# Optimization experiments

Measured on AMD Instinct MI355X. Metric: run time of the kernel, lower is better.

Reference implementation:

```python
import jax, jax.numpy as jnp
import numpy as np

B, S, D, H = 4, 2048, 1024, 16
DK = D // H
THETA = 10000.0


def _rope(x, pos):
    # x: [..., S, DK]; interleaved-pair rotation as in the torch module
    dk = x.shape[-1]
    inv_freq = 1.0 / (THETA ** (jnp.arange(0, dk, 2, dtype=jnp.float32) / dk))  # [dk/2]
    freqs = pos.astype(jnp.float32)[:, None] * inv_freq  # [S, dk/2]
    cos, sin = jnp.cos(freqs), jnp.sin(freqs)
    xr = x.reshape(*x.shape[:-1], dk // 2, 2)
    x0, x1 = xr[..., 0], xr[..., 1]
    rot = jnp.stack([x0 * cos - x1 * sin, x0 * sin + x1 * cos], axis=-1)
    return rot.reshape(x.shape)


def setup_inputs() -> dict:
    key = jax.random.key(0)
    ks = jax.random.split(key, 5)
    scale = 0.02
    return {
        "x": jax.random.normal(ks[0], (B, S, D), dtype=jnp.float32),
        "Wq": jax.random.normal(ks[1], (D, D), dtype=jnp.float32) * scale,
        "Wk": jax.random.normal(ks[2], (D, D), dtype=jnp.float32) * scale,
        "Wv": jax.random.normal(ks[3], (D, D), dtype=jnp.float32) * scale,
        "Wo": jax.random.normal(ks[4], (D, D), dtype=jnp.float32) * scale,
    }


def reference(x, Wq, Wk, Wv, Wo):
    b, s, d = x.shape
    pos = jnp.arange(s)
    # projections (Linear with no bias, y = x @ W^T)
    q = jnp.einsum('bsd,ed->bse', x, Wq).reshape(b, s, H, DK).transpose(0, 2, 1, 3)
    k = jnp.einsum('bsd,ed->bse', x, Wk).reshape(b, s, H, DK).transpose(0, 2, 1, 3)
    v = jnp.einsum('bsd,ed->bse', x, Wv).reshape(b, s, H, DK).transpose(0, 2, 1, 3)
    q = _rope(q, pos)
    k = _rope(k, pos)
    scores = jnp.einsum('bhqd,bhkd->bhqk', q, k) / jnp.sqrt(jnp.float32(DK))
    causal = jnp.tril(jnp.ones((s, s), dtype=bool))
    scores = jnp.where(causal, scores, -jnp.inf)
    attn = jax.nn.softmax(scores, axis=-1)
    out = jnp.einsum('bhqk,bhkd->bhqd', attn, v)
    out = out.transpose(0, 2, 1, 3).reshape(b, s, d)
    return jnp.einsum('bsd,ed->bse', out, Wo)
```

## Files before the change

kernel.cpp:

```cpp
#include <hip/hip_runtime.h>

#define B_  4
#define S_  2048
#define D_  1024
#define H_  16
#define DK_ 64
#define BH_ (B_*H_)
#define L2E 1.44269504088896f

typedef __attribute__((ext_vector_type(8))) short bf16x8;
typedef __attribute__((ext_vector_type(4))) float f32x4;
typedef __attribute__((ext_vector_type(16))) float f32x16;
typedef __attribute__((ext_vector_type(4))) unsigned u32x4;
typedef unsigned short u16;

__device__ __forceinline__ u16 f2bf(float f){
  unsigned u = __builtin_bit_cast(unsigned, f);
  u += 0x7fffu + ((u >> 16) & 1u);
  return (u16)(u >> 16);
}
__device__ __forceinline__ float bf2f(u16 h){
  unsigned u = ((unsigned)h) << 16;
  return __builtin_bit_cast(float, u);
}

#define GLD16(g,l) __builtin_amdgcn_global_load_lds( \
    (const __attribute__((address_space(1))) void*)(g), \
    (__attribute__((address_space(3))) void*)(l), 16, 0, 0)

#define MFMA16(a,b,c) __builtin_amdgcn_mfma_f32_16x16x32_bf16((a),(b),(c),0,0,0)
#define MFMA32(a,b,c) __builtin_amdgcn_mfma_f32_32x32x16_bf16((a),(b),(c),0,0,0)

__global__ void cast_kernel(const float4* __restrict__ in, ushort4* __restrict__ out, int n4){
  int i = blockIdx.x*blockDim.x + threadIdx.x;
  int stride = gridDim.x*blockDim.x;
  for (; i < n4; i += stride){
    float4 v = in[i];
    ushort4 o;
    o.x = f2bf(v.x); o.y = f2bf(v.y); o.z = f2bf(v.z); o.w = f2bf(v.w);
    out[i] = o;
  }
}

__global__ void trig_kernel(float* __restrict__ ct, float* __restrict__ st){
  int t = blockIdx.x*blockDim.x + threadIdx.x;
  int i = t & 31, s = t >> 5;
  float expo = -(float)(2*i) * (1.0f/(float)DK_);
  float inv = powf(10000.0f, expo);
  float ang = (float)s * inv;
  ct[t] = cosf(ang);
  st[t] = sinf(ang);
}

template<int MODE>
__global__ __launch_bounds__(256, 2)
void gemm_bt(const u16* __restrict__ A,
             const u16* __restrict__ B0, const u16* __restrict__ B1, const u16* __restrict__ B2,
             u16* __restrict__ O0, u16* __restrict__ O1, u16* __restrict__ O2,
             float* __restrict__ Cf,
             const float* __restrict__ ct, const float* __restrict__ st, int K){
  __shared__ __align__(16) u16 lAB[2*128*64];
  u16* const lA = lAB;
  u16* const lB = lAB + 128*64;
  const u16* Bm = B0;
  u16* Om = O0;
  if (MODE == 0){
    if (blockIdx.z == 1){ Bm = B1; Om = O1; }
    else if (blockIdx.z == 2){ Bm = B2; Om = O2; }
  }
  const int m0 = blockIdx.y*128, n0 = blockIdx.x*128;
  const int tid = threadIdx.x, wave = tid>>6, lane = tid&63;
  const int wm = wave>>1, wn = wave&1;
  const int srow = lane>>3, scol = (lane&7)*8;

  f32x4 acc[4][4];
  #pragma unroll
  for (int m=0;m<4;++m)
    #pragma unroll
    for (int n=0;n<4;++n) acc[m][n] = (f32x4){0.f,0.f,0.f,0.f};

  #pragma unroll 1
  for (int k0 = 0; k0 < K; k0 += 64){
    #pragma unroll
    for (int j=0;j<4;++j){
      int rb = (wave*4 + j)*8;
      GLD16(A  + (size_t)(m0 + rb + srow)*K + k0 + scol, lA + rb*64);
      GLD16(Bm + (size_t)(n0 + rb + srow)*K + k0 + scol, lB + rb*64);
    }
    __syncthreads();
    #pragma unroll
    for (int kk=0;kk<2;++kk){
      bf16x8 af[4], bfr[4];
      #pragma unroll
      for (int m=0;m<4;++m) af[m]  = *(const bf16x8*)&lA[(wm*64 + m*16 + (lane&15))*64 + kk*32 + (lane>>4)*8];
      #pragma unroll
      for (int n=0;n<4;++n) bfr[n] = *(const bf16x8*)&lB[(wn*64 + n*16 + (lane&15))*64 + kk*32 + (lane>>4)*8];
      #pragma unroll
      for (int m=0;m<4;++m)
        #pragma unroll
        for (int n=0;n<4;++n)
          acc[m][n] = MFMA16(af[m], bfr[n], acc[m][n]);
    }
    __syncthreads();
  }

  if (MODE == 0 && blockIdx.z != 2){
    const float scale = (blockIdx.z == 0) ? 0.125f : 1.0f;
    #pragma unroll
    for (int m=0;m<4;++m){
      const int lr0 = wm*64 + m*16 + ((lane>>4)<<2);
      #pragma unroll
      for (int n=0;n<4;++n){
        const int lc = wn*64 + n*16 + (lane&15);
        #pragma unroll
        for (int r=0;r<4;++r){
          const int lr = lr0 + r;
          lAB[lr*128 + (lc ^ (((lr>>2)&7)<<4))] = f2bf(acc[m][n][r]);
        }
      }
    }
    __syncthreads();
    #pragma unroll
    for (int k=0;k<8;++k){
      const int cid = k*256 + tid;
      const int rr = cid >> 4, cc = cid & 15;
      bf16x8 v = *(const bf16x8*)&lAB[rr*128 + ((cc*8) ^ (((rr>>2)&7)<<4))];
      const int i = m0 + rr, bb = i >> 11, s = i & (S_-1);
      const int e0 = n0 + cc*8, h = e0 >> 6, dk0 = e0 & 63;
      const float4 c4 = *(const float4*)(ct + s*32 + (dk0>>1));
      const float4 s4 = *(const float4*)(st + s*32 + (dk0>>1));
      const float cc4[4] = {c4.x,c4.y,c4.z,c4.w};
      const float ss4[4] = {s4.x,s4.y,s4.z,s4.w};
      bf16x8 o;
      #pragma unroll
      for (int j=0;j<4;++j){
        const float x0 = bf2f((u16)v[2*j]);
        const float x1 = bf2f((u16)v[2*j+1]);
        o[2*j]   = (short)f2bf((x0*cc4[j] - x1*ss4[j])*scale);
        o[2*j+1] = (short)f2bf((x0*ss4[j] + x1*cc4[j])*scale);
      }
      *(bf16x8*)(Om + ((size_t)((bb*H_ + h)*S_ + s))*DK_ + dk0) = o;
    }
  } else {
    #pragma unroll
    for (int m=0;m<4;++m){
      const int rb = m0 + wm*64 + m*16 + ((lane>>4)<<2);
      #pragma unroll
      for (int n=0;n<4;++n){
        const int e = n0 + wn*64 + n*16 + (lane&15);
        if (MODE == 0){
          const int h = e>>6, dk = e&63;
          const int b = rb >> 11, s0 = rb & (S_-1);
          ushort4 w4;
          w4.x = f2bf(acc[m][n][0]); w4.y = f2bf(acc[m][n][1]);
          w4.z = f2bf(acc[m][n][2]); w4.w = f2bf(acc[m][n][3]);
          *(ushort4*)(Om + ((size_t)((b*H_ + h)*DK_ + dk))*S_ + s0) = w4;
        } else {
          #pragma unroll
          for (int r=0;r<4;++r)
            Cf[(size_t)(rb + r)*D_ + e] = acc[m][n][r];
        }
      }
    }
  }
}

__global__ __launch_bounds__(256, 4)
void attn_kernel(const u16* __restrict__ Q, const u16* __restrict__ K,
                 const u16* __restrict__ Vt, u16* __restrict__ O){
  __shared__ __align__(16) u16 lK[2][64*64];
  __shared__ __align__(16) u16 lV[2][64*64];

  const int bh = blockIdx.x;
  const int qt = (int)(gridDim.y - 1 - blockIdx.y);
  const int b = bh >> 4, h = bh & 15;
  const int tid = threadIdx.x, wave = tid>>6, lane = tid&63;
  const int hi = lane >> 5, l31 = lane & 31;
  const int q0 = qt*128, qw = q0 + wave*32;
  const int qg = qw + l31;
  const u16* Qb = Q  + (size_t)bh*S_*DK_;
  const u16* Kb = K  + (size_t)bh*S_*DK_;
  const u16* Vb = Vt + (size_t)bh*DK_*S_;

  bf16x8 qf[4];
  #pragma unroll
  for (int ds=0; ds<4; ++ds)
    qf[ds] = *(const bf16x8*)(Qb + (size_t)qg*DK_ + ds*16 + hi*8);

  f32x16 oacc[2];
  oacc[0] = (f32x16)0.f; oacc[1] = (f32x16)0.f;
  float m_run = -1e30f, l_run = 0.f;

  const int srow8 = lane >> 3;
  const int csw = ((lane&7) ^ srow8) << 3;

  const int kv_end = (qt+1)*128;

  #pragma unroll
  for (int it=0; it<2; ++it){
    const int rb = (it*4 + wave)*8;
    const int row = rb + srow8;
    GLD16(Kb + (size_t)row*DK_ + csw, lK[0] + rb*64);
    GLD16(Vb + (size_t)row*S_ + csw,  lV[0] + rb*64);
  }
  __syncthreads();

  int cur = 0;
  for (int kv0 = 0; kv0 < kv_end; kv0 += 64){
    const int nxt = kv0 + 64;
    if (nxt < kv_end){
      #pragma unroll
      for (int it=0; it<2; ++it){
        const int rb = (it*4 + wave)*8;
        const int row = rb + srow8;
        GLD16(Kb + (size_t)(nxt+row)*DK_ + csw, lK[cur^1] + rb*64);
        GLD16(Vb + (size_t)row*S_ + nxt + csw,  lV[cur^1] + rb*64);
      }
    }

    if (kv0 < qw + 32){
      f32x16 sacc[2];
      sacc[0] = (f32x16)0.f; sacc[1] = (f32x16)0.f;
      __builtin_amdgcn_s_setprio(1);
      #pragma unroll
      for (int kb=0; kb<2; ++kb){
        const int krow = kb*32 + l31;
        #pragma unroll
        for (int ds=0; ds<4; ++ds){
          bf16x8 kf = *(const bf16x8*)&lK[cur][krow*64 + (((ds*2+hi) ^ (krow&7))<<3)];
          sacc[kb] = MFMA32(kf, qf[ds], sacc[kb]);
        }
      }
      __builtin_amdgcn_s_setprio(0);

      if (kv0 + 63 > qw){
        #pragma unroll
        for (int kb=0; kb<2; ++kb)
          #pragma unroll
          for (int r=0; r<16; ++r){
            const int kvg = kv0 + kb*32 + 4*hi + (r&3) + 8*(r>>2);
            if (kvg > qg) sacc[kb][r] = -1e30f;
          }
      }

      float mx = sacc[0][0];
      #pragma unroll
      for (int r=1; r<16; ++r) mx = fmaxf(mx, sacc[0][r]);
      #pragma unroll
      for (int r=0; r<16; ++r) mx = fmaxf(mx, sacc[1][r]);
      mx = fmaxf(mx, __shfl_xor(mx, 32));
      if (!__all((mx - m_run)*L2E <= 8.0f)){
        const float mn = fmaxf(m_run, mx);
        const float alpha = exp2f((m_run - mn)*L2E);
        m_run = mn;
        l_run *= alpha;
        oacc[0] *= alpha;
        oacc[1] *= alpha;
      }
      const float nc = m_run * L2E;
      float ps = 0.f;
      #pragma unroll
      for (int kb=0; kb<2; ++kb)
        #pragma unroll
        for (int r=0; r<16; ++r){
          float v = exp2f(__builtin_fmaf(sacc[kb][r], L2E, -nc));
          sacc[kb][r] = v;
          ps += v;
        }
      ps += __shfl_xor(ps, 32);
      l_run += ps;

      bf16x8 pa[4];
      #pragma unroll
      for (int kb=0; kb<2; ++kb){
        unsigned w[8];
        #pragma unroll
        for (int i=0; i<8; ++i){
          float a = sacc[kb][2*i], b2 = sacc[kb][2*i+1];
          asm("v_cvt_pk_bf16_f32 %0, %1, %2" : "=v"(w[i]) : "v"(a), "v"(b2));
        }
        auto s02 = __builtin_amdgcn_permlane32_swap(w[0], w[2], false, false);
        auto s13 = __builtin_amdgcn_permlane32_swap(w[1], w[3], false, false);
        auto s46 = __builtin_amdgcn_permlane32_swap(w[4], w[6], false, false);
        auto s57 = __builtin_amdgcn_permlane32_swap(w[5], w[7], false, false);
        u32x4 ua = {s02[0], s13[0], s02[1], s13[1]};
        u32x4 ub = {s46[0], s57[0], s46[1], s57[1]};
        pa[kb*2+0] = __builtin_bit_cast(bf16x8, ua);
        pa[kb*2+1] = __builtin_bit_cast(bf16x8, ub);
      }

      __builtin_amdgcn_s_setprio(1);
      #pragma unroll
      for (int dkb=0; dkb<2; ++dkb){
        const int vrow = dkb*32 + l31;
        #pragma unroll
        for (int ks=0; ks<4; ++ks){
          bf16x8 vf = *(const bf16x8*)&lV[cur][vrow*64 + (((ks*2+hi) ^ (vrow&7))<<3)];
          oacc[dkb] = MFMA32(vf, pa[ks], oacc[dkb]);
        }
      }
      __builtin_amdgcn_s_setprio(0);
    }
    __syncthreads();
    cur ^= 1;
  }

  const float inv = 1.0f / l_run;
  #pragma unroll
  for (int dkb=0; dkb<2; ++dkb)
    #pragma unroll
    for (int rq=0; rq<4; ++rq){
      ushort4 w4;
      w4.x = f2bf(oacc[dkb][rq*4+0]*inv);
      w4.y = f2bf(oacc[dkb][rq*4+1]*inv);
      w4.z = f2bf(oacc[dkb][rq*4+2]*inv);
      w4.w = f2bf(oacc[dkb][rq*4+3]*inv);
      const int dk0 = dkb*32 + 8*rq + 4*hi;
      *(ushort4*)(O + (size_t)(b*S_+qg)*D_ + h*DK_ + dk0) = w4;
    }
}

extern "C" void kernel_launch(void* const* d_in, const int* in_sizes, int n_in,
                              void* d_out, int out_size, void* d_ws, size_t ws_size,
                              hipStream_t stream){
  const float* x  = (const float*)d_in[0];
  const float* Wq = (const float*)d_in[1];
  const float* Wk = (const float*)d_in[2];
  const float* Wv = (const float*)d_in[3];
  const float* Wo = (const float*)d_in[4];
  float* out = (float*)d_out;
  char* ws = (char*)d_ws;

  size_t off = 0;
  u16* xb  = (u16*)(ws + off); off += (size_t)B_*S_*D_*2;
  u16* wqb = (u16*)(ws + off); off += (size_t)D_*D_*2;
  u16* wkb = (u16*)(ws + off); off += (size_t)D_*D_*2;
  u16* wvb = (u16*)(ws + off); off += (size_t)D_*D_*2;
  u16* wob = (u16*)(ws + off); off += (size_t)D_*D_*2;
  u16* Qb  = (u16*)(ws + off); off += (size_t)BH_*S_*DK_*2;
  u16* Kb  = (u16*)(ws + off); off += (size_t)BH_*S_*DK_*2;
  u16* Vtb = (u16*)(ws + off); off += (size_t)BH_*S_*DK_*2;
  u16* Ob  = (u16*)(ws + off); off += (size_t)B_*S_*D_*2;
  float* ct = (float*)(ws + off); off += (size_t)S_*32*4;
  float* st = (float*)(ws + off); off += (size_t)S_*32*4;

  cast_kernel<<<2048,256,0,stream>>>((const float4*)x,  (ushort4*)xb,  B_*S_*D_/4);
  cast_kernel<<<512, 256,0,stream>>>((const float4*)Wq, (ushort4*)wqb, D_*D_/4);
  cast_kernel<<<512, 256,0,stream>>>((const float4*)Wk, (ushort4*)wkb, D_*D_/4);
  cast_kernel<<<512, 256,0,stream>>>((const float4*)Wv, (ushort4*)wvb, D_*D_/4);
  cast_kernel<<<512, 256,0,stream>>>((const float4*)Wo, (ushort4*)wob, D_*D_/4);
  trig_kernel<<<(S_*32)/256,256,0,stream>>>(ct, st);

  gemm_bt<0><<<dim3(8,64,3),256,0,stream>>>(xb, wqb,wkb,wvb, Qb,Kb,Vtb, nullptr, ct, st, D_);

  attn_kernel<<<dim3(BH_, S_/128),256,0,stream>>>(Qb, Kb, Vtb, Ob);

  gemm_bt<1><<<dim3(8,64,1),256,0,stream>>>(Ob, wob,wob,wob, nullptr,nullptr,nullptr, out, nullptr, nullptr, D_);
}
```

Baseline: 198.6 us.

## Double-buffer GEMM LDS loads, remap blocks for XCD locality, fuse weight casts

The projection GEMM now double-buffers its LDS tiles: it issues the async global-to-LDS loads for the next K slice before computing on the current one, and drops one barrier per iteration. The 3D grid becomes a flat 1D grid whose block ids are remapped so that consecutive ids spread across the 8 XCDs in contiguous chunks, which should improve L2 reuse. The four weight-cast launches are merged into one kernel, relying on wqb, wkb, wvb and wob being laid out contiguously in the workspace. LDS use doubles to 64 KB per block, which may limit occupancy under the 2-blocks-per-CU launch bound.

```diff
diff --git a/kernel.cpp b/kernel.cpp
--- a/kernel.cpp
+++ b/kernel.cpp
@@ -42,6 +42,22 @@
   }
 }
 
+__global__ void cast4_kernel(const float4* __restrict__ w0, const float4* __restrict__ w1,
+                             const float4* __restrict__ w2, const float4* __restrict__ w3,
+                             ushort4* __restrict__ out){
+  const int per = D_*D_/4;
+  int i = blockIdx.x*blockDim.x + threadIdx.x;
+  int stride = gridDim.x*blockDim.x;
+  for (; i < 4*per; i += stride){
+    int m = i / per, r = i - m*per;
+    const float4* src = (m==0)?w0:(m==1)?w1:(m==2)?w2:w3;
+    float4 v = src[r];
+    ushort4 o;
+    o.x = f2bf(v.x); o.y = f2bf(v.y); o.z = f2bf(v.z); o.w = f2bf(v.w);
+    out[i] = o;
+  }
+}
+
 __global__ void trig_kernel(float* __restrict__ ct, float* __restrict__ st){
   int t = blockIdx.x*blockDim.x + threadIdx.x;
   int i = t & 31, s = t >> 5;
@@ -59,16 +75,21 @@
              u16* __restrict__ O0, u16* __restrict__ O1, u16* __restrict__ O2,
              float* __restrict__ Cf,
              const float* __restrict__ ct, const float* __restrict__ st, int K){
-  __shared__ __align__(16) u16 lAB[2*128*64];
-  u16* const lA = lAB;
-  u16* const lB = lAB + 128*64;
+  __shared__ __align__(16) u16 lds[32768];
+
+  const int id = (int)blockIdx.x;
+  const int nchunk = (MODE==0) ? 192 : 64;
+  const int swz = (id & 7)*nchunk + (id >> 3);
+  int z = 0, rem = swz;
+  if (MODE == 0){ z = swz >> 9; rem = swz & 511; }
+  const int m0 = (rem >> 3) * 128, n0 = (rem & 7) * 128;
+
   const u16* Bm = B0;
   u16* Om = O0;
   if (MODE == 0){
-    if (blockIdx.z == 1){ Bm = B1; Om = O1; }
-    else if (blockIdx.z == 2){ Bm = B2; Om = O2; }
-  }
-  const int m0 = blockIdx.y*128, n0 = blockIdx.x*128;
+    if (z == 1){ Bm = B1; Om = O1; }
+    else if (z == 2){ Bm = B2; Om = O2; }
+  }
   const int tid = threadIdx.x, wave = tid>>6, lane = tid&63;
   const int wm = wave>>1, wn = wave&1;
   const int srow = lane>>3, scol = (lane&7)*8;
@@ -79,15 +100,25 @@
     #pragma unroll
     for (int n=0;n<4;++n) acc[m][n] = (f32x4){0.f,0.f,0.f,0.f};
 
+  #define STAGE(kk0,b) { \
+    u16* sA = lds + (b)*16384; \
+    u16* sB = sA + 8192; \
+    _Pragma("unroll") \
+    for (int j=0;j<4;++j){ \
+      int rb = (wave*4 + j)*8; \
+      GLD16(A  + (size_t)(m0 + rb + srow)*K + (kk0) + scol, sA + rb*64); \
+      GLD16(Bm + (size_t)(n0 + rb + srow)*K + (kk0) + scol, sB + rb*64); \
+    } }
+
+  STAGE(0, 0);
+  __syncthreads();
+
+  int cur = 0;
   #pragma unroll 1
   for (int k0 = 0; k0 < K; k0 += 64){
-    #pragma unroll
-    for (int j=0;j<4;++j){
-      int rb = (wave*4 + j)*8;
-      GLD16(A  + (size_t)(m0 + rb + srow)*K + k0 + scol, lA + rb*64);
-      GLD16(Bm + (size_t)(n0 + rb + srow)*K + k0 + scol, lB + rb*64);
-    }
-    __syncthreads();
+    if (k0 + 64 < K) STAGE(k0 + 64, cur^1);
+    const u16* lA = lds + cur*16384;
+    const u16* lB = lA + 8192;
     #pragma unroll
     for (int kk=0;kk<2;++kk){
       bf16x8 af[4], bfr[4];
@@ -102,10 +133,12 @@
           acc[m][n] = MFMA16(af[m], bfr[n], acc[m][n]);
     }
     __syncthreads();
-  }
-
-  if (MODE == 0 && blockIdx.z != 2){
-    const float scale = (blockIdx.z == 0) ? 0.125f : 1.0f;
+    cur ^= 1;
+  }
+  #undef STAGE
+
+  if (MODE == 0 && z != 2){
+    const float scale = (z == 0) ? 0.125f : 1.0f;
     #pragma unroll
     for (int m=0;m<4;++m){
       const int lr0 = wm*64 + m*16 + ((lane>>4)<<2);
@@ -115,7 +148,7 @@
         #pragma unroll
         for (int r=0;r<4;++r){
           const int lr = lr0 + r;
-          lAB[lr*128 + (lc ^ (((lr>>2)&7)<<4))] = f2bf(acc[m][n][r]);
+          lds[lr*128 + (lc ^ (((lr>>2)&7)<<4))] = f2bf(acc[m][n][r]);
         }
       }
     }
@@ -124,7 +157,7 @@
     for (int k=0;k<8;++k){
       const int cid = k*256 + tid;
       const int rr = cid >> 4, cc = cid & 15;
-      bf16x8 v = *(const bf16x8*)&lAB[rr*128 + ((cc*8) ^ (((rr>>2)&7)<<4))];
+      bf16x8 v = *(const bf16x8*)&lds[rr*128 + ((cc*8) ^ (((rr>>2)&7)<<4))];
       const int i = m0 + rr, bb = i >> 11, s = i & (S_-1);
       const int e0 = n0 + cc*8, h = e0 >> 6, dk0 = e0 & 63;
       const float4 c4 = *(const float4*)(ct + s*32 + (dk0>>1));
@@ -345,15 +378,13 @@
   float* st = (float*)(ws + off); off += (size_t)S_*32*4;
 
   cast_kernel<<<2048,256,0,stream>>>((const float4*)x,  (ushort4*)xb,  B_*S_*D_/4);
-  cast_kernel<<<512, 256,0,stream>>>((const float4*)Wq, (ushort4*)wqb, D_*D_/4);
-  cast_kernel<<<512, 256,0,stream>>>((const float4*)Wk, (ushort4*)wkb, D_*D_/4);
-  cast_kernel<<<512, 256,0,stream>>>((const float4*)Wv, (ushort4*)wvb, D_*D_/4);
-  cast_kernel<<<512, 256,0,stream>>>((const float4*)Wo, (ushort4*)wob, D_*D_/4);
+  cast4_kernel<<<1024,256,0,stream>>>((const float4*)Wq, (const float4*)Wk,
+                                      (const float4*)Wv, (const float4*)Wo, (ushort4*)wqb);
   trig_kernel<<<(S_*32)/256,256,0,stream>>>(ct, st);
 
-  gemm_bt<0><<<dim3(8,64,3),256,0,stream>>>(xb, wqb,wkb,wvb, Qb,Kb,Vtb, nullptr, ct, st, D_);
+  gemm_bt<0><<<1536,256,0,stream>>>(xb, wqb,wkb,wvb, Qb,Kb,Vtb, nullptr, ct, st, D_);
 
   attn_kernel<<<dim3(BH_, S_/128),256,0,stream>>>(Qb, Kb, Vtb, Ob);
 
-  gemm_bt<1><<<dim3(8,64,1),256,0,stream>>>(Ob, wob,wob,wob, nullptr,nullptr,nullptr, out, nullptr, nullptr, D_);
-}
+  gemm_bt<1><<<512,256,0,stream>>>(Ob, wob,wob,wob, nullptr,nullptr,nullptr, out, nullptr, nullptr, D_);
+}
```

New measurement: 185.0 us. -6.9%, faster.
